# Performance work log

Measured on AMD Instinct MI355X. Metric: run time of the kernel, lower is better.

Reference implementation:

```python
import jax, jax.numpy as jnp
import numpy as np

EPS = 1e-7  # keras backend epsilon
ROUTINGS = 3

def squash(s, axis=-1):
    # v = ||s||^2/(1+||s||^2) * s/||s||
    sq = jnp.sum(jnp.square(s), axis=axis, keepdims=True)
    scale = sq / (1.0 + sq) / jnp.sqrt(sq + EPS)
    return scale * s

def setup_inputs() -> dict:
    key = jax.random.key(0)
    k1, k2 = jax.random.split(key)
    B, in_num, in_dim = 64, 2048, 16
    num_caps, dim_caps = 64, 32
    inputs = jax.random.normal(k1, (B, in_num, in_dim), dtype=jnp.float32)
    # glorot_uniform limit = sqrt(6/(fan_in+fan_out)) with fan_in=in_dim, fan_out=dim_caps
    limit = np.sqrt(6.0 / (in_dim + dim_caps)).astype(np.float32)
    W = jax.random.uniform(k2, (num_caps, in_num, dim_caps, in_dim),
                           dtype=jnp.float32, minval=-limit, maxval=limit)
    return {"inputs": inputs, "W": W}

def reference(inputs, W):
    # inputs: [b, i, l]; W: [j, i, k, l]
    # inputs_hat[b, j, i, k] = W[j, i, k, :] @ inputs[b, i, :]
    u_hat = jnp.einsum('jikl,bil->bjik', W, inputs)
    B, J, I, K = u_hat.shape
    b = jnp.zeros((B, J, I), dtype=u_hat.dtype)  # routing logits
    v = None
    for r in range(ROUTINGS):
        c = jax.nn.softmax(b, axis=1)                      # softmax over output capsules j
        s = jnp.einsum('bji,bjik->bjk', c, u_hat)          # weighted sum over input capsules
        v = squash(s)                                      # [b, j, k]
        if r < ROUTINGS - 1:
            b = b + jnp.einsum('bjk,bjik->bji', v, u_hat)  # agreement update
    return v  # [B, num_capsule, dim_capsule]
```

## Files before the change

### kernel.cpp

```cpp
#include <hip/hip_runtime.h>


#define B_ 64
#define I_ 2048
#define L_ 16
#define J_ 64
#define K_ 32
#define N_ 2048

typedef _Float16 half8_t __attribute__((ext_vector_type(8)));
typedef float f32x16 __attribute__((ext_vector_type(16)));
typedef float float4_t __attribute__((ext_vector_type(4)));

__device__ __forceinline__ f32x16 fzero16() {
    f32x16 z;
#pragma unroll
    for (int r = 0; r < 16; ++r) z[r] = 0.f;
    return z;
}

__global__ __launch_bounds__(256) void cast_x_kernel(const float* __restrict__ X,
                                                     _Float16* __restrict__ Xh) {
    unsigned tid = blockIdx.x * 256u + threadIdx.x;
    unsigned b = tid & 63u;
    unsigned i = tid >> 6;
    const float4_t* src = (const float4_t*)(X + (size_t)(b * I_ + i) * L_);
    float4_t f0 = src[0], f1 = src[1], f2 = src[2], f3 = src[3];
    half8_t h0, h1;
#pragma unroll
    for (int e = 0; e < 4; ++e) {
        h0[e] = (_Float16)f0[e];
        h0[4 + e] = (_Float16)f1[e];
        h1[e] = (_Float16)f2[e];
        h1[4 + e] = (_Float16)f3[e];
    }
    _Float16* dst = Xh + (size_t)(i * B_ + b) * L_;
    *(half8_t*)dst = h0;
    *(half8_t*)(dst + 8) = h1;
}

__global__ __launch_bounds__(512) void zcalc_kernel(const _Float16* __restrict__ Wh,
                                                    const _Float16* __restrict__ Xh,
                                                    const _Float16* __restrict__ wvz,
                                                    _Float16* __restrict__ ebuf,
                                                    int SCH, int ICH) {
    const int tid = threadIdx.x;
    const int w = tid >> 6;
    const int l = tid & 63;
    const int h2 = l >> 5;
    const int kb = l & 31;
    const int chunk = blockIdx.x >> 3;
    const int jq = blockIdx.x & 7;
    const int j = jq * 8 + w;

    const _Float16* wp = wvz + ((size_t)(j * 2 + h2) * B_ + kb) * 16;
    const half8_t wv00 = *(const half8_t*)wp;
    const half8_t wv01 = *(const half8_t*)(wp + 8);
    const half8_t wv10 = *(const half8_t*)(wp + 512);
    const half8_t wv11 = *(const half8_t*)(wp + 520);

    const int i0 = chunk * ICH;
#pragma unroll 2
    for (int ii = 0; ii < ICH; ++ii) {
        const int i = i0 + ii;
        const _Float16* xb = Xh + (size_t)i * (B_ * L_);
        half8_t xf0 = *(const half8_t*)(xb + kb * L_ + 8 * h2);
        half8_t xf1 = *(const half8_t*)(xb + (32 + kb) * L_ + 8 * h2);
        half8_t af = *(const half8_t*)(Wh + ((size_t)(i * J_ + j) * K_ + kb) * L_ + 8 * h2);
        f32x16 acc0 = __builtin_amdgcn_mfma_f32_32x32x16_f16(af, xf0, fzero16(), 0, 0, 0);
        f32x16 acc1 = __builtin_amdgcn_mfma_f32_32x32x16_f16(af, xf1, fzero16(), 0, 0, 0);
        float z0 = 0.f, z1 = 0.f;
#pragma unroll
        for (int r = 0; r < 16; ++r) {
            const float a = (r < 8) ? (float)wv00[r] : (float)wv01[r - 8];
            const float b = (r < 8) ? (float)wv10[r] : (float)wv11[r - 8];
            z0 += acc0[r] * a;
            z1 += acc1[r] * b;
        }
        z0 += __shfl_xor(z0, 32, 64);
        z1 += __shfl_xor(z1, 32, 64);
        const float zf = fminf((l < 32) ? z0 : z1, 11.0f);
        ebuf[((size_t)j * I_ + i) * B_ + l] = (_Float16)__expf(zf);
    }
}

__global__ __launch_bounds__(256) void dsum_kernel(const _Float16* __restrict__ ebuf,
                                                   float* __restrict__ rD) {
    const int w = threadIdx.x >> 6;
    const int l = threadIdx.x & 63;
    const int i = blockIdx.x * 4 + w;
    float s = 0.f;
#pragma unroll
    for (int j = 0; j < J_; ++j) s += (float)ebuf[((size_t)j * I_ + i) * B_ + l];
    rD[i * B_ + l] = 1.0f / s;
}

template <int UNIFORM, int CAST>
__global__ __launch_bounds__(512) void s_kernel(const float* __restrict__ Wf,
                                                const _Float16* __restrict__ Wh_in,
                                                _Float16* __restrict__ Wh_out,
                                                const _Float16* __restrict__ Xh,
                                                const _Float16* __restrict__ ebuf,
                                                const float* __restrict__ rD,
                                                _Float16* __restrict__ parts,
                                                int SCH, int ICH) {
    const int tid = threadIdx.x;
    const int w = tid >> 6;
    const int l = tid & 63;
    const int h2 = l >> 5;
    const int kb = l & 31;
    const int chunk = blockIdx.x >> 3;
    const int jq = blockIdx.x & 7;
    const int j = jq * 8 + w;

    float s0[16], s1[16];
#pragma unroll
    for (int r = 0; r < 16; ++r) { s0[r] = 0.f; s1[r] = 0.f; }

    const int i0 = chunk * ICH;
    for (int ii = 0; ii < ICH; ++ii) {
        const int i = i0 + ii;
        const _Float16* xb = Xh + (size_t)i * (B_ * L_);
        half8_t xf0 = *(const half8_t*)(xb + kb * L_ + 8 * h2);
        half8_t xf1 = *(const half8_t*)(xb + (32 + kb) * L_ + 8 * h2);
        half8_t af;
        if (CAST) {
            const float4_t* wsrc =
                (const float4_t*)(Wf + ((size_t)(j * I_ + i) * K_ + kb) * L_ + 8 * h2);
            float4_t a0 = wsrc[0], a1 = wsrc[1];
#pragma unroll
            for (int e = 0; e < 4; ++e) {
                af[e] = (_Float16)a0[e];
                af[4 + e] = (_Float16)a1[e];
            }
            *(half8_t*)(Wh_out + ((size_t)(i * J_ + j) * K_ + kb) * L_ + 8 * h2) = af;
        } else {
            af = *(const half8_t*)(Wh_in + ((size_t)(i * J_ + j) * K_ + kb) * L_ + 8 * h2);
        }
        f32x16 acc0 = __builtin_amdgcn_mfma_f32_32x32x16_f16(af, xf0, fzero16(), 0, 0, 0);
        f32x16 acc1 = __builtin_amdgcn_mfma_f32_32x32x16_f16(af, xf1, fzero16(), 0, 0, 0);
        float c0 = 1.f, c1 = 1.f;
        if (!UNIFORM) {
            const _Float16* ep = ebuf + ((size_t)j * I_ + i) * B_;
            c0 = (float)ep[kb] * rD[i * B_ + kb];
            c1 = (float)ep[32 + kb] * rD[i * B_ + 32 + kb];
        }
#pragma unroll
        for (int r = 0; r < 16; ++r) {
            s0[r] += c0 * acc0[r];
            s1[r] += c1 * acc1[r];
        }
    }
#pragma unroll
    for (int r = 0; r < 16; ++r) {
        const int k = (r & 3) + 8 * (r >> 2) + 4 * h2;
        const size_t n = (size_t)j * K_ + k;
        parts[((size_t)kb * SCH + chunk) * N_ + n] = (_Float16)s0[r];
        parts[((size_t)(32 + kb) * SCH + chunk) * N_ + n] = (_Float16)s1[r];
    }
}

__global__ __launch_bounds__(256) void reduce_kernel(const _Float16* __restrict__ parts,
                                                     _Float16* __restrict__ wvz,
                                                     float* __restrict__ out,
                                                     int SCH, int STEP) {
    const int b = blockIdx.x >> 3;
    const int s = blockIdx.x & 7;
    const int t = threadIdx.x;
    const int n = s * 256 + t;
    const int k = n & 31;
    const int j = n >> 5;
    float acc = 0.f;
    for (int ch = 0; ch < SCH; ++ch) acc += (float)parts[((size_t)b * SCH + ch) * N_ + n];
    if (STEP == 0) acc *= (1.0f / 64.0f);
    float sq = acc * acc;
#pragma unroll
    for (int m = 1; m < 32; m <<= 1) sq += __shfl_xor(sq, m, 64);
    const float scale = sq / (1.0f + sq) / sqrtf(sq + 1e-7f);
    const float v = acc * scale;
    if (STEP == 2) {
        out[(size_t)b * N_ + n] = v;
    } else {
        const int h2 = (k >> 2) & 1;
        const int r = (k & 3) + 4 * (k >> 3);
        const size_t idx = ((size_t)(j * 2 + h2) * B_ + b) * 16 + r;
        const float prev = (STEP == 0) ? 0.f : (float)wvz[idx];
        wvz[idx] = (_Float16)(prev + v);
    }
}

extern "C" void kernel_launch(void* const* d_in, const int* in_sizes, int n_in,
                              void* d_out, int out_size, void* d_ws, size_t ws_size,
                              hipStream_t stream) {
    const float* X = (const float*)d_in[0];
    const float* W = (const float*)d_in[1];
    float* out = (float*)d_out;
    char* ws = (char*)d_ws;

    const size_t WH_BYTES = (size_t)I_ * J_ * K_ * L_ * 2;
    const size_t XH_BYTES = (size_t)I_ * B_ * L_ * 2;
    const size_t WVZ_BYTES = (size_t)J_ * 2 * B_ * 16 * 2;
    const size_t EB_BYTES = (size_t)J_ * I_ * B_ * 2;
    const size_t RD_BYTES = (size_t)I_ * B_ * 4;
    const size_t FIX = WH_BYTES + XH_BYTES + WVZ_BYTES + EB_BYTES + RD_BYTES;

    int SCH = 64;
    if (ws_size < FIX + (size_t)B_ * 64 * N_ * 2) SCH = 32;
    if (ws_size < FIX + (size_t)B_ * 32 * N_ * 2) SCH = 16;
    const int ICH = I_ / SCH;

    _Float16* Wh = (_Float16*)ws;
    _Float16* Xh = (_Float16*)(ws + WH_BYTES);
    _Float16* wvz = (_Float16*)(ws + WH_BYTES + XH_BYTES);
    _Float16* ebuf = (_Float16*)(ws + WH_BYTES + XH_BYTES + WVZ_BYTES);
    float* rD = (float*)(ws + WH_BYTES + XH_BYTES + WVZ_BYTES + EB_BYTES);
    _Float16* parts = (_Float16*)(ws + FIX);

    cast_x_kernel<<<dim3((B_ * I_) / 256), dim3(256), 0, stream>>>(X, Xh);

    s_kernel<1, 1><<<dim3(SCH * 8), dim3(512), 0, stream>>>(W, nullptr, Wh, Xh, nullptr,
                                                            nullptr, parts, SCH, ICH);
    reduce_kernel<<<dim3(B_ * 8), dim3(256), 0, stream>>>(parts, wvz, out, SCH, 0);

    zcalc_kernel<<<dim3(SCH * 8), dim3(512), 0, stream>>>(Wh, Xh, wvz, ebuf, SCH, ICH);
    dsum_kernel<<<dim3(I_ / 4), dim3(256), 0, stream>>>(ebuf, rD);
    s_kernel<0, 0><<<dim3(SCH * 8), dim3(512), 0, stream>>>(nullptr, Wh, nullptr, Xh, ebuf,
                                                            rD, parts, SCH, ICH);
    reduce_kernel<<<dim3(B_ * 8), dim3(256), 0, stream>>>(parts, wvz, out, SCH, 1);

    zcalc_kernel<<<dim3(SCH * 8), dim3(512), 0, stream>>>(Wh, Xh, wvz, ebuf, SCH, ICH);
    dsum_kernel<<<dim3(I_ / 4), dim3(256), 0, stream>>>(ebuf, rD);
    s_kernel<0, 0><<<dim3(SCH * 8), dim3(512), 0, stream>>>(nullptr, Wh, nullptr, Xh, ebuf,
                                                            rD, parts, SCH, ICH);
    reduce_kernel<<<dim3(B_ * 8), dim3(256), 0, stream>>>(parts, wvz, out, SCH, 2);

    (void)in_sizes; (void)n_in; (void)out_size;
}
```

Before: 290.3 us.

## Batch loads across four input capsules, relayout partial sums, restructure reduction

The zcalc and s kernels now load operands for four input capsules up front before issuing their MFMAs, which gives more loads in flight and hides memory latency. The partial-sum buffer is laid out by [chunk][j][k][b], and the reduce kernel runs one block per output capsule, summing squares across k through shared memory instead of wave shuffles. Dot-product and dsum accumulations are split across several independent accumulators to shorten dependency chains. The first routing pass gets its own cast kernel without the uniform-coefficient branch. In exchange, register pressure rises, and the reduce launch has only 64 blocks, which may underuse the GPU.

```diff
diff --git a/kernel.cpp b/kernel.cpp
--- a/kernel.cpp
+++ b/kernel.cpp
@@ -37,6 +37,57 @@
     _Float16* dst = Xh + (size_t)(i * B_ + b) * L_;
     *(half8_t*)dst = h0;
     *(half8_t*)(dst + 8) = h1;
+}
+
+__global__ __launch_bounds__(512) void s0_cast_kernel(const float* __restrict__ Wf,
+                                                      _Float16* __restrict__ Wh_out,
+                                                      const _Float16* __restrict__ Xh,
+                                                      _Float16* __restrict__ parts,
+                                                      int SCH, int ICH) {
+    const int tid = threadIdx.x;
+    const int w = tid >> 6;
+    const int l = tid & 63;
+    const int h2 = l >> 5;
+    const int kb = l & 31;
+    const int chunk = blockIdx.x >> 3;
+    const int jq = blockIdx.x & 7;
+    const int j = jq * 8 + w;
+
+    float s0[16], s1[16];
+#pragma unroll
+    for (int r = 0; r < 16; ++r) { s0[r] = 0.f; s1[r] = 0.f; }
+
+    const int i0 = chunk * ICH;
+    for (int ii = 0; ii < ICH; ++ii) {
+        const int i = i0 + ii;
+        const _Float16* xb = Xh + (size_t)i * (B_ * L_);
+        half8_t xf0 = *(const half8_t*)(xb + kb * L_ + 8 * h2);
+        half8_t xf1 = *(const half8_t*)(xb + (32 + kb) * L_ + 8 * h2);
+        const float4_t* wsrc =
+            (const float4_t*)(Wf + ((size_t)(j * I_ + i) * K_ + kb) * L_ + 8 * h2);
+        float4_t a0 = wsrc[0], a1 = wsrc[1];
+        half8_t af;
+#pragma unroll
+        for (int e = 0; e < 4; ++e) {
+            af[e] = (_Float16)a0[e];
+            af[4 + e] = (_Float16)a1[e];
+        }
+        *(half8_t*)(Wh_out + ((size_t)(i * J_ + j) * K_ + kb) * L_ + 8 * h2) = af;
+        f32x16 acc0 = __builtin_amdgcn_mfma_f32_32x32x16_f16(af, xf0, fzero16(), 0, 0, 0);
+        f32x16 acc1 = __builtin_amdgcn_mfma_f32_32x32x16_f16(af, xf1, fzero16(), 0, 0, 0);
+#pragma unroll
+        for (int r = 0; r < 16; ++r) {
+            s0[r] += acc0[r];
+            s1[r] += acc1[r];
+        }
+    }
+#pragma unroll
+    for (int r = 0; r < 16; ++r) {
+        const int k = (r & 3) + 8 * (r >> 2) + 4 * h2;
+        _Float16* p = parts + (((size_t)chunk * J_ + j) * K_ + k) * B_;
+        p[kb] = (_Float16)s0[r];
+        p[32 + kb] = (_Float16)s1[r];
+    }
 }
 
 __global__ __launch_bounds__(512) void zcalc_kernel(const _Float16* __restrict__ Wh,
@@ -60,27 +111,41 @@
     const half8_t wv11 = *(const half8_t*)(wp + 520);
 
     const int i0 = chunk * ICH;
-#pragma unroll 2
-    for (int ii = 0; ii < ICH; ++ii) {
-        const int i = i0 + ii;
-        const _Float16* xb = Xh + (size_t)i * (B_ * L_);
-        half8_t xf0 = *(const half8_t*)(xb + kb * L_ + 8 * h2);
-        half8_t xf1 = *(const half8_t*)(xb + (32 + kb) * L_ + 8 * h2);
-        half8_t af = *(const half8_t*)(Wh + ((size_t)(i * J_ + j) * K_ + kb) * L_ + 8 * h2);
-        f32x16 acc0 = __builtin_amdgcn_mfma_f32_32x32x16_f16(af, xf0, fzero16(), 0, 0, 0);
-        f32x16 acc1 = __builtin_amdgcn_mfma_f32_32x32x16_f16(af, xf1, fzero16(), 0, 0, 0);
-        float z0 = 0.f, z1 = 0.f;
-#pragma unroll
-        for (int r = 0; r < 16; ++r) {
-            const float a = (r < 8) ? (float)wv00[r] : (float)wv01[r - 8];
-            const float b = (r < 8) ? (float)wv10[r] : (float)wv11[r - 8];
-            z0 += acc0[r] * a;
-            z1 += acc1[r] * b;
-        }
-        z0 += __shfl_xor(z0, 32, 64);
-        z1 += __shfl_xor(z1, 32, 64);
-        const float zf = fminf((l < 32) ? z0 : z1, 11.0f);
-        ebuf[((size_t)j * I_ + i) * B_ + l] = (_Float16)__expf(zf);
+    for (int ig = 0; ig < ICH; ig += 4) {
+        half8_t af[4], x0[4], x1[4];
+#pragma unroll
+        for (int q = 0; q < 4; ++q) {
+            const int i = i0 + ig + q;
+            const _Float16* xb = Xh + (size_t)i * (B_ * L_);
+            x0[q] = *(const half8_t*)(xb + kb * L_ + 8 * h2);
+            x1[q] = *(const half8_t*)(xb + (32 + kb) * L_ + 8 * h2);
+            af[q] = *(const half8_t*)(Wh + ((size_t)(i * J_ + j) * K_ + kb) * L_ + 8 * h2);
+        }
+#pragma unroll
+        for (int q = 0; q < 4; ++q) {
+            const int i = i0 + ig + q;
+            f32x16 acc0 = __builtin_amdgcn_mfma_f32_32x32x16_f16(af[q], x0[q], fzero16(), 0, 0, 0);
+            f32x16 acc1 = __builtin_amdgcn_mfma_f32_32x32x16_f16(af[q], x1[q], fzero16(), 0, 0, 0);
+            float z0a = 0.f, z0b = 0.f, z0c = 0.f, z0d = 0.f;
+            float z1a = 0.f, z1b = 0.f, z1c = 0.f, z1d = 0.f;
+#pragma unroll
+            for (int r = 0; r < 4; ++r) {
+                z0a += acc0[r]      * (float)wv00[r];
+                z0b += acc0[r + 4]  * (float)wv00[r + 4];
+                z0c += acc0[r + 8]  * (float)wv01[r];
+                z0d += acc0[r + 12] * (float)wv01[r + 4];
+                z1a += acc1[r]      * (float)wv10[r];
+                z1b += acc1[r + 4]  * (float)wv10[r + 4];
+                z1c += acc1[r + 8]  * (float)wv11[r];
+                z1d += acc1[r + 12] * (float)wv11[r + 4];
+            }
+            float z0 = (z0a + z0b) + (z0c + z0d);
+            float z1 = (z1a + z1b) + (z1c + z1d);
+            z0 += __shfl_xor(z0, 32, 64);
+            z1 += __shfl_xor(z1, 32, 64);
+            const float zf = fminf((l < 32) ? z0 : z1, 11.0f);
+            ebuf[((size_t)j * I_ + i) * B_ + l] = (_Float16)__expf(zf);
+        }
     }
 }
 
@@ -89,16 +154,18 @@
     const int w = threadIdx.x >> 6;
     const int l = threadIdx.x & 63;
     const int i = blockIdx.x * 4 + w;
-    float s = 0.f;
-#pragma unroll
-    for (int j = 0; j < J_; ++j) s += (float)ebuf[((size_t)j * I_ + i) * B_ + l];
-    rD[i * B_ + l] = 1.0f / s;
-}
-
-template <int UNIFORM, int CAST>
-__global__ __launch_bounds__(512) void s_kernel(const float* __restrict__ Wf,
-                                                const _Float16* __restrict__ Wh_in,
-                                                _Float16* __restrict__ Wh_out,
+    float p0 = 0.f, p1 = 0.f, p2 = 0.f, p3 = 0.f;
+#pragma unroll
+    for (int jq = 0; jq < 16; ++jq) {
+        p0 += (float)ebuf[((size_t)(jq * 4 + 0) * I_ + i) * B_ + l];
+        p1 += (float)ebuf[((size_t)(jq * 4 + 1) * I_ + i) * B_ + l];
+        p2 += (float)ebuf[((size_t)(jq * 4 + 2) * I_ + i) * B_ + l];
+        p3 += (float)ebuf[((size_t)(jq * 4 + 3) * I_ + i) * B_ + l];
+    }
+    rD[i * B_ + l] = 1.0f / ((p0 + p1) + (p2 + p3));
+}
+
+__global__ __launch_bounds__(512) void s_kernel(const _Float16* __restrict__ Wh,
                                                 const _Float16* __restrict__ Xh,
                                                 const _Float16* __restrict__ ebuf,
                                                 const float* __restrict__ rD,
@@ -118,74 +185,82 @@
     for (int r = 0; r < 16; ++r) { s0[r] = 0.f; s1[r] = 0.f; }
 
     const int i0 = chunk * ICH;
-    for (int ii = 0; ii < ICH; ++ii) {
-        const int i = i0 + ii;
-        const _Float16* xb = Xh + (size_t)i * (B_ * L_);
-        half8_t xf0 = *(const half8_t*)(xb + kb * L_ + 8 * h2);
-        half8_t xf1 = *(const half8_t*)(xb + (32 + kb) * L_ + 8 * h2);
-        half8_t af;
-        if (CAST) {
-            const float4_t* wsrc =
-                (const float4_t*)(Wf + ((size_t)(j * I_ + i) * K_ + kb) * L_ + 8 * h2);
-            float4_t a0 = wsrc[0], a1 = wsrc[1];
-#pragma unroll
-            for (int e = 0; e < 4; ++e) {
-                af[e] = (_Float16)a0[e];
-                af[4 + e] = (_Float16)a1[e];
+    for (int ig = 0; ig < ICH; ig += 4) {
+        half8_t af[4], x0[4], x1[4];
+        float e0[4], e1[4], d0[4], d1[4];
+#pragma unroll
+        for (int q = 0; q < 4; ++q) {
+            const int i = i0 + ig + q;
+            const _Float16* xb = Xh + (size_t)i * (B_ * L_);
+            x0[q] = *(const half8_t*)(xb + kb * L_ + 8 * h2);
+            x1[q] = *(const half8_t*)(xb + (32 + kb) * L_ + 8 * h2);
+            af[q] = *(const half8_t*)(Wh + ((size_t)(i * J_ + j) * K_ + kb) * L_ + 8 * h2);
+            const _Float16* ep = ebuf + ((size_t)j * I_ + i) * B_;
+            e0[q] = (float)ep[kb];
+            e1[q] = (float)ep[32 + kb];
+            d0[q] = rD[i * B_ + kb];
+            d1[q] = rD[i * B_ + 32 + kb];
+        }
+#pragma unroll
+        for (int q = 0; q < 4; ++q) {
+            f32x16 acc0 = __builtin_amdgcn_mfma_f32_32x32x16_f16(af[q], x0[q], fzero16(), 0, 0, 0);
+            f32x16 acc1 = __builtin_amdgcn_mfma_f32_32x32x16_f16(af[q], x1[q], fzero16(), 0, 0, 0);
+            const float c0 = e0[q] * d0[q];
+            const float c1 = e1[q] * d1[q];
+#pragma unroll
+            for (int r = 0; r < 16; ++r) {
+                s0[r] += c0 * acc0[r];
+                s1[r] += c1 * acc1[r];
             }
-            *(half8_t*)(Wh_out + ((size_t)(i * J_ + j) * K_ + kb) * L_ + 8 * h2) = af;
-        } else {
-            af = *(const half8_t*)(Wh_in + ((size_t)(i * J_ + j) * K_ + kb) * L_ + 8 * h2);
-        }
-        f32x16 acc0 = __builtin_amdgcn_mfma_f32_32x32x16_f16(af, xf0, fzero16(), 0, 0, 0);
-        f32x16 acc1 = __builtin_amdgcn_mfma_f32_32x32x16_f16(af, xf1, fzero16(), 0, 0, 0);
-        float c0 = 1.f, c1 = 1.f;
-        if (!UNIFORM) {
-            const _Float16* ep = ebuf + ((size_t)j * I_ + i) * B_;
-            c0 = (float)ep[kb] * rD[i * B_ + kb];
-            c1 = (float)ep[32 + kb] * rD[i * B_ + 32 + kb];
-        }
-#pragma unroll
-        for (int r = 0; r < 16; ++r) {
-            s0[r] += c0 * acc0[r];
-            s1[r] += c1 * acc1[r];
         }
     }
 #pragma unroll
     for (int r = 0; r < 16; ++r) {
         const int k = (r & 3) + 8 * (r >> 2) + 4 * h2;
-        const size_t n = (size_t)j * K_ + k;
-        parts[((size_t)kb * SCH + chunk) * N_ + n] = (_Float16)s0[r];
-        parts[((size_t)(32 + kb) * SCH + chunk) * N_ + n] = (_Float16)s1[r];
-    }
-}
-
-__global__ __launch_bounds__(256) void reduce_kernel(const _Float16* __restrict__ parts,
+        _Float16* p = parts + (((size_t)chunk * J_ + j) * K_ + k) * B_;
+        p[kb] = (_Float16)s0[r];
+        p[32 + kb] = (_Float16)s1[r];
+    }
+}
+
+__global__ __launch_bounds__(512) void reduce_kernel(const _Float16* __restrict__ parts,
                                                      _Float16* __restrict__ wvz,
                                                      float* __restrict__ out,
                                                      int SCH, int STEP) {
-    const int b = blockIdx.x >> 3;
-    const int s = blockIdx.x & 7;
+    __shared__ float ssql[8][64];
+    const int j = blockIdx.x;
     const int t = threadIdx.x;
-    const int n = s * 256 + t;
-    const int k = n & 31;
-    const int j = n >> 5;
-    float acc = 0.f;
-    for (int ch = 0; ch < SCH; ++ch) acc += (float)parts[((size_t)b * SCH + ch) * N_ + n];
-    if (STEP == 0) acc *= (1.0f / 64.0f);
-    float sq = acc * acc;
-#pragma unroll
-    for (int m = 1; m < 32; m <<= 1) sq += __shfl_xor(sq, m, 64);
+    const int b = t & 63;
+    const int kg = t >> 6;
+
+    float acc[4] = {0.f, 0.f, 0.f, 0.f};
+    for (int ch = 0; ch < SCH; ++ch) {
+        const _Float16* p = parts + (((size_t)ch * J_ + j) * K_ + kg * 4) * B_ + b;
+#pragma unroll
+        for (int q = 0; q < 4; ++q) acc[q] += (float)p[(size_t)q * B_];
+    }
+    if (STEP == 0) {
+#pragma unroll
+        for (int q = 0; q < 4; ++q) acc[q] *= (1.0f / 64.0f);
+    }
+    ssql[kg][b] = acc[0] * acc[0] + acc[1] * acc[1] + acc[2] * acc[2] + acc[3] * acc[3];
+    __syncthreads();
+    float sq = 0.f;
+#pragma unroll
+    for (int g = 0; g < 8; ++g) sq += ssql[g][b];
     const float scale = sq / (1.0f + sq) / sqrtf(sq + 1e-7f);
-    const float v = acc * scale;
+
     if (STEP == 2) {
-        out[(size_t)b * N_ + n] = v;
+#pragma unroll
+        for (int q = 0; q < 4; ++q)
+            out[(size_t)b * N_ + j * K_ + kg * 4 + q] = acc[q] * scale;
     } else {
-        const int h2 = (k >> 2) & 1;
-        const int r = (k & 3) + 4 * (k >> 3);
-        const size_t idx = ((size_t)(j * 2 + h2) * B_ + b) * 16 + r;
-        const float prev = (STEP == 0) ? 0.f : (float)wvz[idx];
-        wvz[idx] = (_Float16)(prev + v);
+        _Float16* wp = wvz + ((size_t)(j * 2 + (kg & 1)) * B_ + b) * 16 + 4 * (kg >> 1);
+#pragma unroll
+        for (int q = 0; q < 4; ++q) {
+            const float prev = (STEP == 0) ? 0.f : (float)wp[q];
+            wp[q] = (_Float16)(prev + acc[q] * scale);
+        }
     }
 }
 
@@ -205,8 +280,8 @@
     const size_t FIX = WH_BYTES + XH_BYTES + WVZ_BYTES + EB_BYTES + RD_BYTES;
 
     int SCH = 64;
-    if (ws_size < FIX + (size_t)B_ * 64 * N_ * 2) SCH = 32;
-    if (ws_size < FIX + (size_t)B_ * 32 * N_ * 2) SCH = 16;
+    if (ws_size < FIX + (size_t)64 * N_ * B_ * 2) SCH = 32;
+    if (ws_size < FIX + (size_t)32 * N_ * B_ * 2) SCH = 16;
     const int ICH = I_ / SCH;
 
     _Float16* Wh = (_Float16*)ws;
@@ -218,21 +293,18 @@
 
     cast_x_kernel<<<dim3((B_ * I_) / 256), dim3(256), 0, stream>>>(X, Xh);
 
-    s_kernel<1, 1><<<dim3(SCH * 8), dim3(512), 0, stream>>>(W, nullptr, Wh, Xh, nullptr,
-                                                            nullptr, parts, SCH, ICH);
-    reduce_kernel<<<dim3(B_ * 8), dim3(256), 0, stream>>>(parts, wvz, out, SCH, 0);
+    s0_cast_kernel<<<dim3(SCH * 8), dim3(512), 0, stream>>>(W, Wh, Xh, parts, SCH, ICH);
+    reduce_kernel<<<dim3(J_), dim3(512), 0, stream>>>(parts, wvz, out, SCH, 0);
 
     zcalc_kernel<<<dim3(SCH * 8), dim3(512), 0, stream>>>(Wh, Xh, wvz, ebuf, SCH, ICH);
     dsum_kernel<<<dim3(I_ / 4), dim3(256), 0, stream>>>(ebuf, rD);
-    s_kernel<0, 0><<<dim3(SCH * 8), dim3(512), 0, stream>>>(nullptr, Wh, nullptr, Xh, ebuf,
-                                                            rD, parts, SCH, ICH);
-    reduce_kernel<<<dim3(B_ * 8), dim3(256), 0, stream>>>(parts, wvz, out, SCH, 1);
+    s_kernel<<<dim3(SCH * 8), dim3(512), 0, stream>>>(Wh, Xh, ebuf, rD, parts, SCH, ICH);
+    reduce_kernel<<<dim3(J_), dim3(512), 0, stream>>>(parts, wvz, out, SCH, 1);
 
     zcalc_kernel<<<dim3(SCH * 8), dim3(512), 0, stream>>>(Wh, Xh, wvz, ebuf, SCH, ICH);
     dsum_kernel<<<dim3(I_ / 4), dim3(256), 0, stream>>>(ebuf, rD);
-    s_kernel<0, 0><<<dim3(SCH * 8), dim3(512), 0, stream>>>(nullptr, Wh, nullptr, Xh, ebuf,
-                                                            rD, parts, SCH, ICH);
-    reduce_kernel<<<dim3(B_ * 8), dim3(256), 0, stream>>>(parts, wvz, out, SCH, 2);
+    s_kernel<<<dim3(SCH * 8), dim3(512), 0, stream>>>(Wh, Xh, ebuf, rD, parts, SCH, ICH);
+    reduce_kernel<<<dim3(J_), dim3(512), 0, stream>>>(parts, wvz, out, SCH, 2);
 
     (void)in_sizes; (void)n_in; (void)out_size;
 }
```

Result: slower. 297.9 us (+2.6%).
